# Kernel tuning notes

Hardware: AMD Instinct MI355X
Metric: run time of the kernel (lower is better)

## Reference

```python
import jax, jax.numpy as jnp
import numpy as np

N = 100000   # nodes
E = 1600000  # edges
IN = 256
H = 128


def gcn_conv(x, W, b, src, dst, n):
    """PyG GCNConv (eval): self-loops + symmetric normalization + linear + scatter-add."""
    h = x @ W                                   # [n, out]
    loop = jnp.arange(n)
    s = jnp.concatenate([src, loop])            # [E+n]
    d = jnp.concatenate([dst, loop])
    deg = jax.ops.segment_sum(jnp.ones_like(d, dtype=h.dtype), d, num_segments=n)
    dinv = jnp.where(deg > 0, jax.lax.rsqrt(deg), 0.0)
    norm = dinv[s] * dinv[d]                    # [E+n]
    out = jax.ops.segment_sum(h[s] * norm[:, None], d, num_segments=n)
    return out + b


def setup_inputs() -> dict:
    key = jax.random.key(0)
    ks = jax.random.split(key, 8)
    x = jax.random.normal(ks[0], (N, IN), dtype=jnp.float32)
    edge_index = jax.random.randint(ks[1], (2, E), 0, N, dtype=jnp.int64)
    W1 = jax.random.normal(ks[2], (IN, H), dtype=jnp.float32) * (1.0 / np.sqrt(IN))
    b1 = jnp.zeros((H,), dtype=jnp.float32)
    W2 = jax.random.normal(ks[3], (H, H), dtype=jnp.float32) * (1.0 / np.sqrt(H))
    b2 = jnp.zeros((H,), dtype=jnp.float32)
    W3 = jax.random.normal(ks[4], (H, H), dtype=jnp.float32) * (1.0 / np.sqrt(H))
    b3 = jnp.zeros((H,), dtype=jnp.float32)
    return {"x": x, "edge_index": edge_index, "W1": W1, "b1": b1,
            "W2": W2, "b2": b2, "W3": W3, "b3": b3}


def reference(x, edge_index, W1, b1, W2, b2, W3, b3):
    src, dst = edge_index[0], edge_index[1]
    n = x.shape[0]
    h = gcn_conv(x, W1, b1, src, dst, n)
    h = jax.nn.relu(h)                          # dropout inactive in eval
    h = gcn_conv(h, W2, b2, src, dst, n)
    h = jax.nn.relu(h)
    h = gcn_conv(h, W3, b3, src, dst, n)
    return h
```

## Files before the change

### kernel.cpp

```cpp
#include <hip/hip_runtime.h>

#define HDIM 128

typedef unsigned int uint;
typedef unsigned short ushort;
typedef __attribute__((ext_vector_type(8))) short short8;
typedef __attribute__((ext_vector_type(4))) float f32x4;

typedef __attribute__((address_space(3))) uint  lds_u32_t;
typedef const __attribute__((address_space(1))) uint g_u32_t;
#define GLDS16(gp, lp) __builtin_amdgcn_global_load_lds((g_u32_t*)(gp), (lds_u32_t*)(lp), 16, 0, 0)

__device__ inline ushort f2bf(float f) {
    uint u = __float_as_uint(f);
    uint rounding = 0x7fffu + ((u >> 16) & 1u);
    return (ushort)((u + rounding) >> 16);
}
__device__ inline float bf2f(ushort h) { return __uint_as_float(((uint)h) << 16); }

__device__ inline float4 bf4_to_f4(uint2 u) {
    float4 r;
    r.x = __uint_as_float(u.x << 16);
    r.y = __uint_as_float(u.x & 0xffff0000u);
    r.z = __uint_as_float(u.y << 16);
    r.w = __uint_as_float(u.y & 0xffff0000u);
    return r;
}


__global__ __launch_bounds__(256) void k_count(const int* __restrict__ dst,
                                               int* __restrict__ cnt,
                                               int* __restrict__ rank, int e) {
    int i = blockIdx.x * 256 + threadIdx.x;
    if (i < e) rank[i] = atomicAdd(&cnt[dst[i]], 1);
}

__global__ __launch_bounds__(256) void k_dinv(const int* __restrict__ cnt,
                                              float* __restrict__ dinv, int n) {
    int i = blockIdx.x * 256 + threadIdx.x;
    if (i < n) dinv[i] = rsqrtf((float)(cnt[i] + 1));
}

__global__ __launch_bounds__(256) void k_scan1(const int* __restrict__ cnt,
                                               int* __restrict__ offs,
                                               int* __restrict__ bsum, int n) {
    __shared__ int sm[256];
    int tid = threadIdx.x;
    int i = blockIdx.x * 256 + tid;
    int v = (i < n) ? cnt[i] : 0;
    sm[tid] = v;
    __syncthreads();
    for (int off = 1; off < 256; off <<= 1) {
        int t = (tid >= off) ? sm[tid - off] : 0;
        __syncthreads();
        sm[tid] += t;
        __syncthreads();
    }
    if (i < n) offs[i] = sm[tid] - v;
    if (tid == 255) bsum[blockIdx.x] = sm[255];
}

__global__ __launch_bounds__(512) void k_scan2(int* __restrict__ bsum, int nb) {
    __shared__ int sm[512];
    int tid = threadIdx.x;
    int v = (tid < nb) ? bsum[tid] : 0;
    sm[tid] = v;
    __syncthreads();
    for (int off = 1; off < 512; off <<= 1) {
        int t = (tid >= off) ? sm[tid - off] : 0;
        __syncthreads();
        sm[tid] += t;
        __syncthreads();
    }
    if (tid < nb) bsum[tid] = sm[tid] - v;
}

__global__ __launch_bounds__(256) void k_scan3(int* __restrict__ offs,
                                               const int* __restrict__ bsum,
                                               int n, int e) {
    int i = blockIdx.x * 256 + threadIdx.x;
    if (i < n) offs[i] += bsum[blockIdx.x];
    if (i == 0) offs[n] = e;
}

__global__ __launch_bounds__(256) void k_fill(const int* __restrict__ src,
                                              const int* __restrict__ dst,
                                              const int* __restrict__ offs,
                                              const int* __restrict__ rank,
                                              int* __restrict__ csr, int e) {
    int i = blockIdx.x * 256 + threadIdx.x;
    if (i < e) {
        csr[offs[dst[i]] + rank[i]] = src[i];
    }
}


__global__ __launch_bounds__(256) void k_prep_w(const float* __restrict__ W,
                                                ushort* __restrict__ wt, int K) {
    int idx = blockIdx.x * 256 + threadIdx.x;
    if (idx < K * HDIM) {
        int k = idx >> 7;
        int c = idx & 127;
        wt[(k >> 5) * 4096 + c * 32 + (k & 31)] = f2bf(W[idx]);
    }
}


template<int NKT>
__global__ __launch_bounds__(512)
void k_mm(const ushort* __restrict__ XP,
          const ushort* __restrict__ WP,
          const float* __restrict__ dinv,
          ushort* __restrict__ g, int n)
{
    __shared__ ushort w[NKT * 4096];

    const int tid  = threadIdx.x;
    const int wv   = tid >> 6;
    const int lane = tid & 63;
    const int r    = lane & 15;
    const int gq   = lane >> 4;

    #pragma unroll
    for (int i = 0; i < NKT; i++) {
        int off = (i * 512 + tid) * 8;
        GLDS16(WP + off, w + off);
    }

    const int tile   = blockIdx.x * 8 + wv;
    const int ntiles = (n + 15) / 16;
    const bool twork = tile < ntiles;
    int rowr = twork ? tile * 16 + r : 0;
    const bool rok = twork && (rowr < n);
    if (twork && rowr >= n) rowr = n - 1;

    const size_t n32 = (size_t)n * 32;

    short8 xc[NKT];
    if (twork) {
        const size_t ro = (size_t)rowr * 32 + gq * 8;
        #pragma unroll
        for (int kt = 0; kt < NKT; kt++)
            xc[kt] = *(const short8*)(XP + kt * n32 + ro);
    }

    __syncthreads();

    if (!twork) return;

    f32x4 acc[8];
    #pragma unroll
    for (int m = 0; m < 8; m++) acc[m] = (f32x4){0.f, 0.f, 0.f, 0.f};

    #pragma unroll
    for (int kt = 0; kt < NKT; kt++) {
        #pragma unroll
        for (int m = 0; m < 8; m++) {
            short8 wf = *(const short8*)&w[kt * 4096 + (m * 16 + r) * 32 + gq * 8];
            acc[m] = __builtin_amdgcn_mfma_f32_16x16x32_bf16(wf, xc[kt], acc[m], 0, 0, 0);
        }
    }

    if (rok) {
        float di = dinv[rowr];
        #pragma unroll
        for (int m = 0; m < 8; m++) {
            f32x4 a = acc[m];
            uint2 pk;
            pk.x = (uint)f2bf(a[0] * di) | ((uint)f2bf(a[1] * di) << 16);
            pk.y = (uint)f2bf(a[2] * di) | ((uint)f2bf(a[3] * di) << 16);
            *(uint2*)(g + (size_t)rowr * HDIM + m * 16 + gq * 4) = pk;
        }
    }
}


__global__ __launch_bounds__(512)
void k_mm_f32(const float* __restrict__ X,
              const ushort* __restrict__ WP,
              const float* __restrict__ dinv,
              ushort* __restrict__ g, int n)
{
    __shared__ ushort w[8 * 4096];

    const int tid  = threadIdx.x;
    const int wv   = tid >> 6;
    const int lane = tid & 63;
    const int r    = lane & 15;
    const int gq   = lane >> 4;

    #pragma unroll
    for (int i = 0; i < 8; i++) {
        int off = (i * 512 + tid) * 8;
        GLDS16(WP + off, w + off);
    }

    const int tile   = blockIdx.x * 8 + wv;
    const int ntiles = (n + 15) / 16;
    const bool twork = tile < ntiles;
    int rowr = twork ? tile * 16 + r : 0;
    const bool rok = twork && (rowr < n);
    if (twork && rowr >= n) rowr = n - 1;

    f32x4 xf[16];
    if (twork) {
        const f32x4* xp = (const f32x4*)(X + (size_t)rowr * 256);
        #pragma unroll
        for (int kt = 0; kt < 8; kt++) {
            xf[kt * 2]     = xp[kt * 8 + gq * 2];
            xf[kt * 2 + 1] = xp[kt * 8 + gq * 2 + 1];
        }
    }

    __syncthreads();

    if (!twork) return;

    f32x4 acc[8];
    #pragma unroll
    for (int m = 0; m < 8; m++) acc[m] = (f32x4){0.f, 0.f, 0.f, 0.f};

    #pragma unroll
    for (int kt = 0; kt < 8; kt++) {
        float v[8] = {xf[kt*2][0], xf[kt*2][1], xf[kt*2][2], xf[kt*2][3],
                      xf[kt*2+1][0], xf[kt*2+1][1], xf[kt*2+1][2], xf[kt*2+1][3]};
        short8 bh;
        #pragma unroll
        for (int q = 0; q < 8; q++) bh[q] = (short)f2bf(v[q]);
        #pragma unroll
        for (int m = 0; m < 8; m++) {
            short8 wf = *(const short8*)&w[kt * 4096 + (m * 16 + r) * 32 + gq * 8];
            acc[m] = __builtin_amdgcn_mfma_f32_16x16x32_bf16(wf, bh, acc[m], 0, 0, 0);
        }
    }

    if (rok) {
        float di = dinv[rowr];
        #pragma unroll
        for (int m = 0; m < 8; m++) {
            f32x4 a = acc[m];
            uint2 pk;
            pk.x = (uint)f2bf(a[0] * di) | ((uint)f2bf(a[1] * di) << 16);
            pk.y = (uint)f2bf(a[2] * di) | ((uint)f2bf(a[3] * di) << 16);
            *(uint2*)(g + (size_t)rowr * HDIM + m * 16 + gq * 4) = pk;
        }
    }
}


template<bool RELU, bool EMIT_PLANE>
__global__ __launch_bounds__(256) void k_gather(const ushort* __restrict__ g,
                                                const int* __restrict__ csr,
                                                const int* __restrict__ offs,
                                                const float* __restrict__ dinv,
                                                const float* __restrict__ bias,
                                                float* __restrict__ out,
                                                ushort* __restrict__ ap, int n)
{
    int t    = blockIdx.x * 256 + threadIdx.x;
    int node = t >> 5;
    int l    = t & 31;
    if (node >= n) return;

    int e0 = offs[node];
    int e1 = offs[node + 1];

    float4 acc = bf4_to_f4(*(const uint2*)(g + (size_t)node * HDIM + l * 4));

    int e = e0;
    for (; e + 4 <= e1; e += 4) {
        int s0 = csr[e], s1 = csr[e + 1], s2 = csr[e + 2], s3 = csr[e + 3];
        float4 v0 = bf4_to_f4(*(const uint2*)(g + (size_t)s0 * HDIM + l * 4));
        float4 v1 = bf4_to_f4(*(const uint2*)(g + (size_t)s1 * HDIM + l * 4));
        float4 v2 = bf4_to_f4(*(const uint2*)(g + (size_t)s2 * HDIM + l * 4));
        float4 v3 = bf4_to_f4(*(const uint2*)(g + (size_t)s3 * HDIM + l * 4));
        acc.x += v0.x + v1.x + v2.x + v3.x;
        acc.y += v0.y + v1.y + v2.y + v3.y;
        acc.z += v0.z + v1.z + v2.z + v3.z;
        acc.w += v0.w + v1.w + v2.w + v3.w;
    }
    for (; e < e1; e++) {
        int s = csr[e];
        float4 v = bf4_to_f4(*(const uint2*)(g + (size_t)s * HDIM + l * 4));
        acc.x += v.x; acc.y += v.y; acc.z += v.z; acc.w += v.w;
    }

    float di  = dinv[node];
    float4 bb = *(const float4*)(bias + l * 4);
    float4 o;
    o.x = fmaf(di, acc.x, bb.x);
    o.y = fmaf(di, acc.y, bb.y);
    o.z = fmaf(di, acc.z, bb.z);
    o.w = fmaf(di, acc.w, bb.w);
    if (RELU) {
        o.x = fmaxf(o.x, 0.f); o.y = fmaxf(o.y, 0.f);
        o.z = fmaxf(o.z, 0.f); o.w = fmaxf(o.w, 0.f);
    }
    if (EMIT_PLANE) {
        uint2 ph;
        ph.x = (uint)f2bf(o.x) | ((uint)f2bf(o.y) << 16);
        ph.y = (uint)f2bf(o.z) | ((uint)f2bf(o.w) << 16);
        size_t base = (size_t)(l >> 3) * ((size_t)n * 32) + (size_t)node * 32 + (l & 7) * 4;
        *(uint2*)(ap + base) = ph;
    } else {
        *(float4*)(out + (size_t)node * HDIM + l * 4) = o;
    }
}


extern "C" void kernel_launch(void* const* d_in, const int* in_sizes, int n_in,
                              void* d_out, int out_size, void* d_ws, size_t ws_size,
                              hipStream_t stream)
{
    const float* x  = (const float*)d_in[0];
    const int*   ei = (const int*)d_in[1];
    const float* W1 = (const float*)d_in[2];
    const float* b1 = (const float*)d_in[3];
    const float* W2 = (const float*)d_in[4];
    const float* b2 = (const float*)d_in[5];
    const float* W3 = (const float*)d_in[6];
    const float* b3 = (const float*)d_in[7];
    float* out = (float*)d_out;

    const int n = in_sizes[0] / 256;
    const int E = in_sizes[1] / 2;
    const int* src = ei;
    const int* dst = ei + E;

    char*   ws   = (char*)d_ws;
    float*  dinv = (float*)(ws);
    int*    cnt  = (int*)(ws + (512 << 10));
    int*    offs = (int*)(ws + (1 << 20));
    int*    bsum = (int*)(ws + 1536 * 1024);
    int*    csr  = (int*)(ws + 1600 * 1024);
    int*    rank = (int*)(ws + (size_t)(8 << 20));
    ushort* wt   = (ushort*)(ws + 14848 * 1024);
    ushort* g    = (ushort*)(ws + (size_t)(16 << 20));
    ushort* xp   = (ushort*)(ws + (size_t)(42 << 20));

    dim3 blk(256);
    int ngrid = (n + 255) / 256;
    int egrid = (E + 255) / 256;

    hipMemsetAsync(cnt, 0, (size_t)n * 4, stream);
    k_count<<<egrid, blk, 0, stream>>>(dst, cnt, rank, E);
    k_dinv<<<ngrid, blk, 0, stream>>>(cnt, dinv, n);
    k_scan1<<<ngrid, blk, 0, stream>>>(cnt, offs, bsum, n);
    k_scan2<<<1, 512, 0, stream>>>(bsum, ngrid);
    k_scan3<<<ngrid, blk, 0, stream>>>(offs, bsum, n, E);
    k_fill<<<egrid, blk, 0, stream>>>(src, dst, offs, rank, csr, E);

    int ntiles   = (n + 15) / 16;
    int mm_grid  = (ntiles + 7) / 8;
    int gat_grid = (int)(((size_t)n * 32 + 255) / 256);

    k_prep_w<<<(256 * HDIM + 255) / 256, blk, 0, stream>>>(W1, wt, 256);
    k_mm_f32<<<mm_grid, 512, 0, stream>>>(x, wt, dinv, g, n);
    k_gather<true, true><<<gat_grid, blk, 0, stream>>>(g, csr, offs, dinv, b1, nullptr, xp, n);
    k_prep_w<<<(128 * HDIM + 255) / 256, blk, 0, stream>>>(W2, wt, 128);
    k_mm<4><<<mm_grid, 512, 0, stream>>>(xp, wt, dinv, g, n);
    k_gather<true, true><<<gat_grid, blk, 0, stream>>>(g, csr, offs, dinv, b2, nullptr, xp, n);
    k_prep_w<<<(128 * HDIM + 255) / 256, blk, 0, stream>>>(W3, wt, 128);
    k_mm<4><<<mm_grid, 512, 0, stream>>>(xp, wt, dinv, g, n);
    k_gather<false, false><<<gat_grid, blk, 0, stream>>>(g, csr, offs, dinv, b3, out, nullptr, n);
}
```

Baseline: 367.2 us.

## Privatize degree counters into 16 copies to cut atomic contention in CSR build

Degree counting now spreads atomics over 16 private counter arrays chosen by block index, and the scan builds per-copy offsets interleaved per node so the fill can place edges without a global counter. The dinv kernel is folded into the first scan pass. This targets contention on the same-address atomics in k_count, at the cost of a 16x larger counter memset, a 16x larger offset array, and strided reads in the scan.

New measurement: 385.3 us. 1.05x slower.

```diff
diff --git a/kernel.cpp b/kernel.cpp
--- a/kernel.cpp
+++ b/kernel.cpp
@@ -30,33 +30,40 @@
 
 __global__ __launch_bounds__(256) void k_count(const int* __restrict__ dst,
                                                int* __restrict__ cnt,
-                                               int* __restrict__ rank, int e) {
+                                               int* __restrict__ rank,
+                                               int e, int n) {
     int i = blockIdx.x * 256 + threadIdx.x;
-    if (i < e) rank[i] = atomicAdd(&cnt[dst[i]], 1);
-}
-
-__global__ __launch_bounds__(256) void k_dinv(const int* __restrict__ cnt,
-                                              float* __restrict__ dinv, int n) {
-    int i = blockIdx.x * 256 + threadIdx.x;
-    if (i < n) dinv[i] = rsqrtf((float)(cnt[i] + 1));
+    int c = blockIdx.x & 15;
+    if (i < e) rank[i] = atomicAdd(&cnt[(size_t)c * n + dst[i]], 1);
 }
 
 __global__ __launch_bounds__(256) void k_scan1(const int* __restrict__ cnt,
-                                               int* __restrict__ offs,
-                                               int* __restrict__ bsum, int n) {
+                                               int* __restrict__ offs2,
+                                               int* __restrict__ bsum,
+                                               float* __restrict__ dinv, int n) {
     __shared__ int sm[256];
     int tid = threadIdx.x;
-    int i = blockIdx.x * 256 + tid;
-    int v = (i < n) ? cnt[i] : 0;
-    sm[tid] = v;
+    int d = blockIdx.x * 256 + tid;
+    int vals[16];
+    int total = 0;
+    if (d < n) {
+        #pragma unroll
+        for (int c = 0; c < 16; c++) { vals[c] = cnt[(size_t)c * n + d]; total += vals[c]; }
+    }
+    sm[tid] = total;
     __syncthreads();
     for (int off = 1; off < 256; off <<= 1) {
-        int t = (tid >= off) ? sm[tid - off] : 0;
+        int t2 = (tid >= off) ? sm[tid - off] : 0;
         __syncthreads();
-        sm[tid] += t;
+        sm[tid] += t2;
         __syncthreads();
     }
-    if (i < n) offs[i] = sm[tid] - v;
+    if (d < n) {
+        int run = sm[tid] - total;
+        #pragma unroll
+        for (int c = 0; c < 16; c++) { offs2[d * 16 + c] = run; run += vals[c]; }
+        dinv[d] = rsqrtf((float)(total + 1));
+    }
     if (tid == 255) bsum[blockIdx.x] = sm[255];
 }
 
@@ -75,22 +82,23 @@
     if (tid < nb) bsum[tid] = sm[tid] - v;
 }
 
-__global__ __launch_bounds__(256) void k_scan3(int* __restrict__ offs,
+__global__ __launch_bounds__(256) void k_scan3(int* __restrict__ offs2,
                                                const int* __restrict__ bsum,
                                                int n, int e) {
-    int i = blockIdx.x * 256 + threadIdx.x;
-    if (i < n) offs[i] += bsum[blockIdx.x];
-    if (i == 0) offs[n] = e;
+    int j = blockIdx.x * 256 + threadIdx.x;
+    if (j < n * 16) offs2[j] += bsum[j >> 12];
+    if (j == 0) offs2[n * 16] = e;
 }
 
 __global__ __launch_bounds__(256) void k_fill(const int* __restrict__ src,
                                               const int* __restrict__ dst,
-                                              const int* __restrict__ offs,
+                                              const int* __restrict__ offs2,
                                               const int* __restrict__ rank,
                                               int* __restrict__ csr, int e) {
     int i = blockIdx.x * 256 + threadIdx.x;
+    int c = blockIdx.x & 15;
     if (i < e) {
-        csr[offs[dst[i]] + rank[i]] = src[i];
+        csr[offs2[dst[i] * 16 + c] + rank[i]] = src[i];
     }
 }
 
@@ -251,7 +259,7 @@
 template<bool RELU, bool EMIT_PLANE>
 __global__ __launch_bounds__(256) void k_gather(const ushort* __restrict__ g,
                                                 const int* __restrict__ csr,
-                                                const int* __restrict__ offs,
+                                                const int* __restrict__ offs2,
                                                 const float* __restrict__ dinv,
                                                 const float* __restrict__ bias,
                                                 float* __restrict__ out,
@@ -262,8 +270,8 @@
     int l    = t & 31;
     if (node >= n) return;
 
-    int e0 = offs[node];
-    int e1 = offs[node + 1];
+    int e0 = offs2[node << 4];
+    int e1 = offs2[(node + 1) << 4];
 
     float4 acc = bf4_to_f4(*(const uint2*)(g + (size_t)node * HDIM + l * 4));
 
@@ -327,28 +335,28 @@
     const int* src = ei;
     const int* dst = ei + E;
 
-    char*   ws   = (char*)d_ws;
-    float*  dinv = (float*)(ws);
-    int*    cnt  = (int*)(ws + (512 << 10));
-    int*    offs = (int*)(ws + (1 << 20));
-    int*    bsum = (int*)(ws + 1536 * 1024);
-    int*    csr  = (int*)(ws + 1600 * 1024);
-    int*    rank = (int*)(ws + (size_t)(8 << 20));
-    ushort* wt   = (ushort*)(ws + 14848 * 1024);
-    ushort* g    = (ushort*)(ws + (size_t)(16 << 20));
-    ushort* xp   = (ushort*)(ws + (size_t)(42 << 20));
+    char*   ws    = (char*)d_ws;
+    float*  dinv  = (float*)(ws);
+    int*    bsum  = (int*)(ws + (512 << 10));
+    ushort* wt    = (ushort*)(ws + (768 << 10));
+    int*    cnt   = (int*)(ws + (size_t)(1 << 20));
+    int*    offs2 = (int*)(ws + (size_t)(8 << 20));
+    int*    csr   = (int*)(ws + (size_t)(16 << 20));
+    int*    rank  = (int*)(ws + (size_t)(24 << 20));
+    ushort* g     = (ushort*)(ws + (size_t)(32 << 20));
+    ushort* xp    = (ushort*)(ws + (size_t)(64 << 20));
 
     dim3 blk(256);
     int ngrid = (n + 255) / 256;
     int egrid = (E + 255) / 256;
-
-    hipMemsetAsync(cnt, 0, (size_t)n * 4, stream);
-    k_count<<<egrid, blk, 0, stream>>>(dst, cnt, rank, E);
-    k_dinv<<<ngrid, blk, 0, stream>>>(cnt, dinv, n);
-    k_scan1<<<ngrid, blk, 0, stream>>>(cnt, offs, bsum, n);
+    int s3grid = (n * 16 + 255) / 256;
+
+    hipMemsetAsync(cnt, 0, (size_t)n * 16 * 4, stream);
+    k_count<<<egrid, blk, 0, stream>>>(dst, cnt, rank, E, n);
+    k_scan1<<<ngrid, blk, 0, stream>>>(cnt, offs2, bsum, dinv, n);
     k_scan2<<<1, 512, 0, stream>>>(bsum, ngrid);
-    k_scan3<<<ngrid, blk, 0, stream>>>(offs, bsum, n, E);
-    k_fill<<<egrid, blk, 0, stream>>>(src, dst, offs, rank, csr, E);
+    k_scan3<<<s3grid, blk, 0, stream>>>(offs2, bsum, n, E);
+    k_fill<<<egrid, blk, 0, stream>>>(src, dst, offs2, rank, csr, E);
 
     int ntiles   = (n + 15) / 16;
     int mm_grid  = (ntiles + 7) / 8;
@@ -356,11 +364,11 @@
 
     k_prep_w<<<(256 * HDIM + 255) / 256, blk, 0, stream>>>(W1, wt, 256);
     k_mm_f32<<<mm_grid, 512, 0, stream>>>(x, wt, dinv, g, n);
-    k_gather<true, true><<<gat_grid, blk, 0, stream>>>(g, csr, offs, dinv, b1, nullptr, xp, n);
+    k_gather<true, true><<<gat_grid, blk, 0, stream>>>(g, csr, offs2, dinv, b1, nullptr, xp, n);
     k_prep_w<<<(128 * HDIM + 255) / 256, blk, 0, stream>>>(W2, wt, 128);
     k_mm<4><<<mm_grid, 512, 0, stream>>>(xp, wt, dinv, g, n);
-    k_gather<true, true><<<gat_grid, blk, 0, stream>>>(g, csr, offs, dinv, b2, nullptr, xp, n);
+    k_gather<true, true><<<gat_grid, blk, 0, stream>>>(g, csr, offs2, dinv, b2, nullptr, xp, n);
     k_prep_w<<<(128 * HDIM + 255) / 256, blk, 0, stream>>>(W3, wt, 128);
     k_mm<4><<<mm_grid, 512, 0, stream>>>(xp, wt, dinv, g, n);
-    k_gather<false, false><<<gat_grid, blk, 0, stream>>>(g, csr, offs, dinv, b3, out, nullptr, n);
-}
+    k_gather<false, false><<<gat_grid, blk, 0, stream>>>(g, csr, offs2, dinv, b3, out, nullptr, n);
+}
```
